# Kernel optimization log

Measured on AMD Instinct MI355X. Metric: run time of the kernel, lower is better.

Reference implementation:

```python
import jax, jax.numpy as jnp
import numpy as np

N, T, D_KQ, E_KQ, D_V, E_V, H = 2, 2048, 1024, 1024, 1024, 1024, 16


def setup_inputs() -> dict:
    key = jax.random.key(0)
    ks = jax.random.split(key, 12)
    def lin(k, fan_in, fan_out):
        return jax.random.normal(k, (fan_in, fan_out), jnp.float32) * (1.0 / np.sqrt(fan_in))
    return {
        "kq": jax.random.normal(ks[0], (N, T, D_KQ), jnp.float32),
        "v": jax.random.normal(ks[1], (N, T, D_V), jnp.float32),
        "Wk": lin(ks[2], D_KQ, E_KQ), "bk": jnp.zeros((E_KQ,), jnp.float32),
        "Wq": lin(ks[3], D_KQ, E_KQ), "bq": jnp.zeros((E_KQ,), jnp.float32),
        "Wv": lin(ks[4], D_V, E_V),   "bv": jnp.zeros((E_V,), jnp.float32),
        "W1": lin(ks[5], E_V, 4 * E_V), "b1": jnp.zeros((4 * E_V,), jnp.float32),
        "W2": lin(ks[6], 4 * E_V, E_V), "b2": jnp.zeros((E_V,), jnp.float32),
    }


def _shifted_causal_mask(T):
    # triu(-inf, diagonal=0): block j >= i (strictly-past attention), except [0,0] unmasked
    row = jnp.arange(T)[:, None]
    col = jnp.arange(T)[None, :]
    mask = jnp.where(col < row, 0.0, -jnp.inf).astype(jnp.float32)
    return mask.at[0, 0].set(0.0)


def reference(kq, v, Wk, bk, Wq, bq, Wv, bv, W1, b1, W2, b2):
    n, T, _ = kq.shape
    hd_kq = E_KQ // H
    hd_v = E_V // H
    # projections -> [n, H, T, hd]
    k = (kq @ Wk + bk).reshape(n, T, H, hd_kq).transpose(0, 2, 1, 3)
    q = (kq @ Wq + bq).reshape(n, T, H, hd_kq).transpose(0, 2, 1, 3)
    vv = (v @ Wv + bv).reshape(n, T, H, hd_v).transpose(0, 2, 1, 3)
    # NOTE: no 1/sqrt(d) scaling, faithful to source
    scores = jnp.einsum("bhqd,bhkd->bhqk", q, k) + _shifted_causal_mask(T)
    attn = jax.nn.softmax(scores, axis=-1)
    out = jnp.einsum("bhqk,bhkd->bhqd", attn, vv)
    out = out.transpose(0, 2, 1, 3).reshape(n, T, E_V)
    # GELU FFN (torch nn.GELU default = exact erf form)
    h = jax.nn.gelu(out @ W1 + b1, approximate=False)
    return h @ W2 + b2
```

## Files before the change

kernel.cpp:

```cpp
#include <hip/hip_runtime.h>

typedef short bf16x8 __attribute__((ext_vector_type(8)));
typedef unsigned short u16x8 __attribute__((ext_vector_type(8)));
typedef float f32x4 __attribute__((ext_vector_type(4)));
typedef unsigned short u16;

#define MFMA16(a, b, c) __builtin_amdgcn_mfma_f32_16x16x32_bf16((a), (b), (c), 0, 0, 0)
#define VMCNT0() asm volatile("s_waitcnt vmcnt(0)" ::: "memory")
#define VMCNTN(n) asm volatile("s_waitcnt vmcnt(" #n ")" ::: "memory")

__device__ __forceinline__ u16 bf16_rtn(float f) {
  unsigned u = __float_as_uint(f);
  u += 0x7fffu + ((u >> 16) & 1u);
  return (u16)(u >> 16);
}
__device__ __forceinline__ float bf16_to_f(u16 h) {
  return __uint_as_float(((unsigned)h) << 16);
}
__device__ __forceinline__ void splitf(float f, u16& hi, u16& lo) {
  hi = bf16_rtn(f);
  lo = bf16_rtn(f - bf16_to_f(hi));
}
__device__ __forceinline__ void gload16(const void* g, void* l) {
  __builtin_amdgcn_global_load_lds(
      (const __attribute__((address_space(1))) unsigned int*)g,
      (__attribute__((address_space(3))) unsigned int*)l, 16, 0, 0);
}
__device__ __forceinline__ float exp2_hw(float x) {
  float r;
  asm("v_exp_f32 %0, %1" : "=v"(r) : "v"(x));
  return r;
}
__device__ __forceinline__ void swz_bid(int& bx, int& by) {
  int gx = gridDim.x;
  int lin = (int)blockIdx.y * gx + (int)blockIdx.x;
  int cpx = (gx * (int)gridDim.y) >> 3;
  int nl = (lin & 7) * cpx + (lin >> 3);
  bx = nl % gx;
  by = nl / gx;
}

__global__ void k_cvt(const float* __restrict__ a, const float* __restrict__ b,
                      u16* __restrict__ ah, u16* __restrict__ vb) {
  int i = blockIdx.x * blockDim.x + threadIdx.x;
  const int N4 = 1 << 20;
  const float4 v4 = (i < N4) ? ((const float4*)a)[i] : ((const float4*)b)[i - N4];
  ushort4 h;
  h.x = bf16_rtn(v4.x);
  h.y = bf16_rtn(v4.y);
  h.z = bf16_rtn(v4.z);
  h.w = bf16_rtn(v4.w);
  if (i < N4)
    ((ushort4*)ah)[i] = h;
  else
    ((ushort4*)vb)[i - N4] = h;
}

__global__ void k_tconvW(const float* __restrict__ Wk, const float* __restrict__ Wq,
                         const float* __restrict__ Wv, u16* __restrict__ hi,
                         u16* __restrict__ lo, u16* __restrict__ wvt) {
  int z = blockIdx.z;
  const float* in = (z == 0) ? Wk : (z == 1) ? Wq : Wv;
  __shared__ float tile[32][33];
  int c0 = blockIdx.x * 32, r0 = blockIdx.y * 32;
  int tx = threadIdx.x & 31, ty = threadIdx.x >> 5;
#pragma unroll
  for (int i = 0; i < 4; ++i)
    tile[ty + i * 8][tx] = in[(size_t)(r0 + ty + i * 8) * 1024 + c0 + tx];
  __syncthreads();
#pragma unroll
  for (int i = 0; i < 4; ++i) {
    float v = tile[tx][ty + i * 8];
    size_t o = (size_t)(c0 + ty + i * 8) * 1024 + r0 + tx;
    if (z < 2) {
      u16 h, l;
      splitf(v, h, l);
      hi[(size_t)z * 1048576 + o] = h;
      lo[(size_t)z * 1048576 + o] = l;
    } else {
      wvt[o] = bf16_rtn(v);
    }
  }
}

__global__ void k_tconv(const float* __restrict__ in, u16* __restrict__ hi,
                        int R, int C) {
  __shared__ float tile[32][33];
  int c0 = blockIdx.x * 32, r0 = blockIdx.y * 32;
  int tx = threadIdx.x & 31, ty = threadIdx.x >> 5;
#pragma unroll
  for (int i = 0; i < 4; ++i)
    tile[ty + i * 8][tx] = in[(size_t)(r0 + ty + i * 8) * C + c0 + tx];
  __syncthreads();
#pragma unroll
  for (int i = 0; i < 4; ++i)
    hi[(size_t)(c0 + ty + i * 8) * R + r0 + tx] = bf16_rtn(tile[tx][ty + i * 8]);
}

template <int GELU, int OUT, int BN>
__global__ __launch_bounds__(256) void k_gemm(
    const u16* __restrict__ A, const u16* __restrict__ B,
    const float* __restrict__ bias, void* __restrict__ C0,
    int M, int Nc, int K) {
  const int NB = BN / 32;
  const int BUFE = 8192 + BN * 64;
  __shared__ u16 sm[3 * BUFE];

  int bx, by;
  swz_bid(bx, by);
  int m0 = by * 128, n0 = bx * BN;
  int t = threadIdx.x, lane = t & 63, w = t >> 6;
  int wr = (w >> 1) * 64, wc = (w & 1) * (BN / 2);
  int li = lane & 15, g = lane >> 4;
  int lrow = lane >> 3, lcg = lane & 7;

  f32x4 acc[4][NB] = {};
  const int nk = K >> 6;

  auto stage = [&](int kb, int buf) {
    int k0 = kb * 64;
    u16* base = sm + buf * BUFE;
#pragma unroll
    for (int j = 0; j < 4; ++j) {
      int jj = w * 4 + j;
      int row = jj * 8 + lrow;
      int cg = lcg ^ (row & 7);
      gload16(A + (size_t)(m0 + row) * K + k0 + cg * 8, base + jj * 512);
    }
#pragma unroll
    for (int j = 0; j < NB; ++j) {
      int jj = w * NB + j;
      int row = jj * 8 + lrow;
      int cg = lcg ^ (row & 7);
      gload16(B + (size_t)(n0 + row) * K + k0 + cg * 8, base + 8192 + jj * 512);
    }
  };

  stage(0, 0);
  stage(1, 1);
  if (NB == 4) { VMCNTN(8); } else { VMCNTN(6); }
  __syncthreads();

  int cur = 0;
  for (int kb = 0; kb < nk; ++kb) {
    int stb = cur + 2;
    if (stb >= 3) stb -= 3;
    if (kb + 2 < nk) stage(kb + 2, stb);

    const u16* bs = sm + cur * BUFE;
#pragma unroll
    for (int kk = 0; kk < 2; ++kk) {
      bf16x8 af[4], bf[NB];
#pragma unroll
      for (int i = 0; i < 4; ++i) {
        int row = wr + i * 16 + li;
        af[i] = *(const bf16x8*)&bs[row * 64 + (((kk * 4 + g) ^ (li & 7)) << 3)];
      }
#pragma unroll
      for (int b = 0; b < NB; ++b) {
        int row = wc + b * 16 + li;
        bf[b] = *(const bf16x8*)&bs[8192 + row * 64 + (((kk * 4 + g) ^ (li & 7)) << 3)];
      }
#pragma unroll
      for (int a = 0; a < 4; ++a)
#pragma unroll
        for (int b = 0; b < NB; ++b) acc[a][b] = MFMA16(af[a], bf[b], acc[a][b]);
    }
    if (kb + 2 < nk) {
      if (NB == 4) { VMCNTN(8); } else { VMCNTN(6); }
    } else {
      VMCNT0();
    }
    __syncthreads();
    cur = (cur == 2) ? 0 : cur + 1;
  }

#pragma unroll
  for (int a = 0; a < 4; ++a)
#pragma unroll
    for (int b = 0; b < NB; ++b)
#pragma unroll
      for (int r = 0; r < 4; ++r) {
        int row = m0 + wr + a * 16 + g * 4 + r;
        int col = n0 + wc + b * 16 + li;
        float v = acc[a][b][r] + bias[col];
        if (GELU) v = 0.5f * v * (1.0f + erff(v * 0.70710678118654752f));
        if (OUT == 0) {
          ((float*)C0)[(size_t)row * Nc + col] = v;
        } else if (OUT == 1) {
          ((u16*)C0)[(size_t)row * Nc + col] = bf16_rtn(v);
        } else if (OUT == 5) {
          int nn = row >> 11, tt = row & 2047, kbb = tt >> 6, tr = tt & 63;
          int hq = col >> 6, d = col & 63;
          size_t base = (((size_t)nn * 16 + hq) * 32 + kbb) * 8192 + 4096;
          size_t ov = base + d * 64 + (tr & 7) + (((tr >> 3) ^ (d & 7)) << 3);
          ((u16*)C0)[ov] = bf16_rtn(v);
        }
      }
}

template <int GELU, int OUT>
__global__ __launch_bounds__(512, 1) void k_gemm2(
    const u16* __restrict__ A, const u16* __restrict__ B,
    const float* __restrict__ bias, void* __restrict__ C0,
    int M, int Nc, int K) {
  const int BUFE = 32768;
  __shared__ u16 sm[2 * BUFE];

  int bx, by;
  swz_bid(bx, by);
  int m0 = by * 256, n0 = bx * 256;
  int t = threadIdx.x, lane = t & 63, w = t >> 6;
  int wr = (w >> 2) * 128, wc = (w & 3) * 64;
  int li = lane & 15, g = lane >> 4;
  int lrow = lane >> 3, lcg = lane & 7;

  f32x4 acc[8][4] = {};
  const int nk = K >> 6;

  auto stage = [&](int kb, int buf) {
    int k0 = kb * 64;
    u16* base = sm + buf * BUFE;
#pragma unroll
    for (int j = 0; j < 4; ++j) {
      int jj = w * 4 + j;
      int row = jj * 8 + lrow;
      int cg = lcg ^ (row & 7);
      gload16(A + (size_t)(m0 + row) * K + k0 + cg * 8, base + jj * 512);
      gload16(B + (size_t)(n0 + row) * K + k0 + cg * 8, base + 16384 + jj * 512);
    }
  };

  stage(0, 0);
  VMCNT0();
  __syncthreads();

  int cur = 0;
  for (int kb = 0; kb < nk; ++kb) {
    if (kb + 1 < nk) stage(kb + 1, cur ^ 1);

    const u16* bs = sm + cur * BUFE;
#pragma unroll
    for (int kk = 0; kk < 2; ++kk) {
      bf16x8 af[8], bf[4];
#pragma unroll
      for (int i = 0; i < 8; ++i) {
        int row = wr + i * 16 + li;
        af[i] = *(const bf16x8*)&bs[row * 64 + (((kk * 4 + g) ^ (li & 7)) << 3)];
      }
#pragma unroll
      for (int b = 0; b < 4; ++b) {
        int row = wc + b * 16 + li;
        bf[b] = *(const bf16x8*)&bs[16384 + row * 64 + (((kk * 4 + g) ^ (li & 7)) << 3)];
      }
#pragma unroll
      for (int a = 0; a < 8; ++a)
#pragma unroll
        for (int b = 0; b < 4; ++b) acc[a][b] = MFMA16(af[a], bf[b], acc[a][b]);
    }
    VMCNT0();
    __syncthreads();
    cur ^= 1;
  }

#pragma unroll
  for (int a = 0; a < 8; ++a)
#pragma unroll
    for (int b = 0; b < 4; ++b)
#pragma unroll
      for (int r = 0; r < 4; ++r) {
        int row = m0 + wr + a * 16 + g * 4 + r;
        int col = n0 + wc + b * 16 + li;
        float v = acc[a][b][r] + bias[col];
        if (GELU) v = 0.5f * v * (1.0f + erff(v * 0.70710678118654752f));
        if (OUT == 1)
          ((u16*)C0)[(size_t)row * Nc + col] = bf16_rtn(v);
        else
          ((float*)C0)[(size_t)row * Nc + col] = v;
      }
}

__global__ __launch_bounds__(256) void k_gemm_s(
    const u16* __restrict__ Ahi, const u16* __restrict__ Bhi,
    const u16* __restrict__ Blo, const float* __restrict__ bias,
    const float* __restrict__ bias2, void* __restrict__ C0,
    void* __restrict__ C1, void* __restrict__ C2, int M, int Nc, int K) {
  const int BUFE = 12288;
  __shared__ u16 sm[3 * BUFE];

  int bx, by;
  swz_bid(bx, by);
  int m0 = by * 128, n0 = bx * 128;
  int t = threadIdx.x, lane = t & 63, w = t >> 6;
  int wr = (w >> 1) * 64, wc = (w & 1) * 64;
  int li = lane & 15, g = lane >> 4;
  int srow = lane >> 2;
  int sc = ((lane & 3) ^ ((srow >> 1) & 3)) * 8;

  f32x4 acc[4][4] = {};
  const int nk = K >> 5;

  auto stage = [&](int kb, int buf) {
    int k0 = kb * 32;
    u16* base = sm + buf * BUFE;
#pragma unroll
    for (int c = 0; c < 2; ++c) {
      int row = w * 32 + c * 16 + srow;
      int ldso = w * 1024 + c * 512;
      gload16(Ahi + (size_t)(m0 + row) * K + k0 + sc, base + ldso);
      gload16(Bhi + (size_t)(n0 + row) * K + k0 + sc, base + 4096 + ldso);
      gload16(Blo + (size_t)(n0 + row) * K + k0 + sc, base + 8192 + ldso);
    }
  };

  stage(0, 0);
  stage(1, 1);
  VMCNTN(6);
  __syncthreads();

  int cur = 0;
  for (int kb = 0; kb < nk; ++kb) {
    int stb = cur + 2;
    if (stb >= 3) stb -= 3;
    if (kb + 2 < nk) stage(kb + 2, stb);

    const u16* bs = sm + cur * BUFE;
    bf16x8 af[4], bfr[4], bfl[4];
#pragma unroll
    for (int i = 0; i < 4; ++i) {
      int swz = (g ^ ((li >> 1) & 3)) << 3;
      af[i] = *(const bf16x8*)&bs[(wr + i * 16 + li) * 32 + swz];
      bfr[i] = *(const bf16x8*)&bs[4096 + (wc + i * 16 + li) * 32 + swz];
      bfl[i] = *(const bf16x8*)&bs[8192 + (wc + i * 16 + li) * 32 + swz];
    }
#pragma unroll
    for (int a = 0; a < 4; ++a)
#pragma unroll
      for (int b = 0; b < 4; ++b) {
        acc[a][b] = MFMA16(af[a], bfr[b], acc[a][b]);
        acc[a][b] = MFMA16(af[a], bfl[b], acc[a][b]);
      }
    if (kb + 2 < nk) {
      VMCNTN(6);
    } else {
      VMCNT0();
    }
    __syncthreads();
    cur = (cur == 2) ? 0 : cur + 1;
  }

#pragma unroll
  for (int a = 0; a < 4; ++a)
#pragma unroll
    for (int b = 0; b < 4; ++b)
#pragma unroll
      for (int r = 0; r < 4; ++r) {
        int row = m0 + wr + a * 16 + g * 4 + r;
        int col = n0 + wc + b * 16 + li;
        float bb = col < 1024 ? bias[col] : bias2[col - 1024];
        float v = acc[a][b][r] + bb;
        if (col < 1024) {
          int nn = row >> 11, tt = row & 2047, kbb = tt >> 6, tr = tt & 63;
          int hq = col >> 6, d = col & 63, ks = d >> 5, dc = d & 31;
          size_t base = (((size_t)nn * 16 + hq) * 32 + kbb) * 8192;
          size_t oh = base + ks * 2048 + tr * 32 + (dc & 7) +
                      (((dc >> 3) ^ ((tr >> 1) & 3)) << 3);
          ((u16*)C0)[oh] = bf16_rtn(v);
        } else {
          int cq = col - 1024;
          float vq = v * 1.4426950408889634f;
          u16 hh, ll;
          splitf(vq, hh, ll);
          size_t off = (((size_t)(row >> 11) * 16 + (cq >> 6)) * 2048 + (row & 2047)) * 64 + (cq & 63);
          ((u16*)C1)[off] = hh;
          ((u16*)C2)[off] = ll;
        }
      }
}

__global__ __launch_bounds__(512) void k_attn(
    const u16* __restrict__ Qh, const u16* __restrict__ Ql,
    const u16* __restrict__ KV, u16* __restrict__ out) {
  const int T = 2048, HD = 64, H = 16, E = 1024;
  int hc = blockIdx.x;
  int h = hc & 15, n = hc >> 4;
  int qq = 15 - (int)blockIdx.y;
  __shared__ u16 KB[3][8192];
  __shared__ u16 P[2][128][36];
  int t = threadIdx.x, lane = t & 63, w = t >> 6;
  int li = lane & 15, g = lane >> 4;

  const size_t nh = (size_t)n * H + h;
  const u16* qhb = Qh + (nh * 2048 + (size_t)qq * 128) * 64;
  const u16* qlb = Ql + (nh * 2048 + (size_t)qq * 128) * 64;
  const u16* kvb = KV + nh * 32 * 8192;

  bf16x8 qh[2], ql[2];
#pragma unroll
  for (int ks = 0; ks < 2; ++ks) {
    qh[ks] = *(const bf16x8*)&qhb[(w * 16 + li) * 64 + ks * 32 + g * 8];
    ql[ks] = *(const bf16x8*)&qlb[(w * 16 + li) * 64 + ks * 32 + g * 8];
  }

#pragma unroll
  for (int j = 0; j < 2; ++j)
    gload16(kvb + (w * 2 + j) * 512 + lane * 8, &KB[0][(w * 2 + j) * 512]);
#pragma unroll
  for (int j = 0; j < 2; ++j)
    gload16(kvb + 8192 + (w * 2 + j) * 512 + lane * 8, &KB[1][(w * 2 + j) * 512]);
  VMCNTN(2);
  __syncthreads();

  float lr[4] = {0.f, 0.f, 0.f, 0.f};
  f32x4 O[4] = {};
  int cur = 0;
  const int nkb = 2 * qq + 2;

  for (int kb = 0; kb < nkb; ++kb) {
    int stb = cur + 2;
    if (stb >= 3) stb -= 3;
    if (kb + 2 < nkb) {
      const u16* src = kvb + (size_t)(kb + 2) * 8192 + (w * 2) * 512 + lane * 8;
#pragma unroll
      for (int j = 0; j < 2; ++j)
        gload16(src + j * 512, &KB[stb][(w * 2 + j) * 512]);
    }

    f32x4 s[4] = {};
#pragma unroll
    for (int ks = 0; ks < 2; ++ks)
#pragma unroll
      for (int c = 0; c < 4; ++c) {
        int jr = c * 16 + li;
        int sw = (jr >> 1) & 3;
        bf16x8 kh = *(const bf16x8*)&KB[cur][ks * 2048 + jr * 32 + ((g ^ sw) << 3)];
        s[c] = MFMA16(qh[ks], kh, s[c]);
        s[c] = MFMA16(ql[ks], kh, s[c]);
      }

    if (kb >= 2 * qq) {
#pragma unroll
      for (int c = 0; c < 4; ++c)
#pragma unroll
        for (int r = 0; r < 4; ++r) {
          int i = qq * 128 + w * 16 + g * 4 + r;
          int j = kb * 64 + c * 16 + li;
          if (!(j < i || (i == 0 && j == 0))) s[c][r] = -INFINITY;
        }
    }

#pragma unroll
    for (int c = 0; c < 4; ++c)
#pragma unroll
      for (int r = 0; r < 4; ++r) {
        float p = exp2_hw(s[c][r]);
        s[c][r] = p;
        lr[r] += p;
      }

#pragma unroll
    for (int c = 0; c < 4; ++c)
#pragma unroll
      for (int r = 0; r < 4; ++r)
        P[c >> 1][w * 16 + g * 4 + r][(c & 1) * 16 + li] = bf16_rtn(s[c][r]);

#pragma unroll
    for (int ks = 0; ks < 2; ++ks) {
      bf16x8 pa = *(const bf16x8*)&P[ks][w * 16 + li][g * 8];
#pragma unroll
      for (int c = 0; c < 4; ++c) {
        int d = c * 16 + li;
        int tc = ks * 4 + g;
        bf16x8 vb = *(const bf16x8*)&KB[cur][4096 + d * 64 + ((tc ^ (d & 7)) << 3)];
        O[c] = MFMA16(pa, vb, O[c]);
      }
    }
    if (kb + 2 < nkb) {
      VMCNTN(2);
    } else {
      VMCNT0();
    }
    __syncthreads();
    cur = (cur == 2) ? 0 : cur + 1;
  }

#pragma unroll
  for (int off = 1; off < 16; off <<= 1)
#pragma unroll
    for (int r = 0; r < 4; ++r) lr[r] += __shfl_xor(lr[r], off, 16);

#pragma unroll
  for (int c = 0; c < 4; ++c)
#pragma unroll
    for (int r = 0; r < 4; ++r) {
      float v = O[c][r] / lr[r];
      size_t row = (size_t)n * T + qq * 128 + w * 16 + g * 4 + r;
      out[row * E + h * HD + c * 16 + li] = bf16_rtn(v);
    }
}

extern "C" void kernel_launch(void* const* d_in, const int* in_sizes, int n_in,
                              void* d_out, int out_size, void* d_ws, size_t ws_size,
                              hipStream_t stream) {
  const float* kq = (const float*)d_in[0];
  const float* v = (const float*)d_in[1];
  const float* Wk = (const float*)d_in[2];
  const float* bk = (const float*)d_in[3];
  const float* Wq = (const float*)d_in[4];
  const float* bq = (const float*)d_in[5];
  const float* Wv = (const float*)d_in[6];
  const float* bv = (const float*)d_in[7];
  const float* W1 = (const float*)d_in[8];
  const float* b1 = (const float*)d_in[9];
  const float* W2 = (const float*)d_in[10];
  const float* b2 = (const float*)d_in[11];
  float* outp = (float*)d_out;

  char* ws = (char*)d_ws;
  u16* kq_hi = (u16*)(ws + 0);
  u16* v_bf = (u16*)(ws + 8388608);
  u16* hbuf = (u16*)(ws + 0);
  u16* WkqT_hi = (u16*)(ws + 33554432);
  u16* WkqT_lo = (u16*)(ws + 37748736);
  u16* WvT = (u16*)(ws + 41943040);
  u16* W1T = (u16*)(ws + 44040192);
  u16* W2T = (u16*)(ws + 52428800);
  u16* Qh = (u16*)(ws + 60817408);
  u16* Ql = (u16*)(ws + 69206016);
  u16* KV = (u16*)(ws + 77594624);
  u16* attn_o = (u16*)(ws + 102760448);

  k_cvt<<<8192, 256, 0, stream>>>(kq, v, kq_hi, v_bf);
  k_tconvW<<<dim3(32, 32, 3), 256, 0, stream>>>(Wk, Wq, Wv, WkqT_hi, WkqT_lo, WvT);
  k_tconv<<<dim3(128, 32), 256, 0, stream>>>(W1, W1T, 1024, 4096);
  k_tconv<<<dim3(32, 128), 256, 0, stream>>>(W2, W2T, 4096, 1024);

  k_gemm_s<<<dim3(16, 32), 256, 0, stream>>>(
      kq_hi, WkqT_hi, WkqT_lo, bk, bq, KV, Qh, Ql, 4096, 2048, 1024);
  k_gemm<0, 5, 64><<<dim3(16, 32), 256, 0, stream>>>(
      v_bf, WvT, bv, KV, 4096, 1024, 1024);

  k_attn<<<dim3(32, 16), 512, 0, stream>>>(Qh, Ql, KV, attn_o);

  k_gemm2<1, 1><<<dim3(16, 16), 512, 0, stream>>>(
      attn_o, W1T, b1, hbuf, 4096, 4096, 1024);
  k_gemm<0, 0, 128><<<dim3(8, 32), 256, 0, stream>>>(
      hbuf, W2T, b2, outp, 4096, 1024, 4096);
}
```

Before: 228.0 us.

## Interleave gemm2 global-to-LDS staging with MFMA phases using barriers and setprio

Splits the next-tile prefetch into four quarter loads issued one per compute phase, and splits each k-step's MFMA work into half-row phases separated by raw s_barrier calls. s_setprio raises wave priority around the MFMA bursts. The aim is to spread memory issue across the compute and let waves overlap loads with matrix math, following the ping-pong style schedule. It adds more barriers per iteration and relies on raw s_barrier without explicit LDS waitcnt, which risks ordering hazards on the ds_reads.

```diff
diff --git a/kernel.cpp b/kernel.cpp
--- a/kernel.cpp
+++ b/kernel.cpp
@@ -218,34 +218,36 @@
   f32x4 acc[8][4] = {};
   const int nk = K >> 6;
 
-  auto stage = [&](int kb, int buf) {
+  auto stageq = [&](int kb, int buf, int q) {
     int k0 = kb * 64;
-    u16* base = sm + buf * BUFE;
-#pragma unroll
-    for (int j = 0; j < 4; ++j) {
-      int jj = w * 4 + j;
+    const u16* src = (q < 2) ? A : B;
+    size_t gr = (size_t)((q < 2) ? m0 : n0) + (q & 1) * 128;
+    u16* nb = sm + buf * BUFE + q * 8192;
+#pragma unroll
+    for (int j = 0; j < 2; ++j) {
+      int jj = w * 2 + j;
       int row = jj * 8 + lrow;
-      int cg = lcg ^ (row & 7);
-      gload16(A + (size_t)(m0 + row) * K + k0 + cg * 8, base + jj * 512);
-      gload16(B + (size_t)(n0 + row) * K + k0 + cg * 8, base + 16384 + jj * 512);
+      int cg = lcg ^ lrow;
+      gload16(src + (gr + row) * K + k0 + cg * 8, nb + jj * 512);
     }
   };
 
-  stage(0, 0);
+#pragma unroll
+  for (int q = 0; q < 4; ++q) stageq(0, 0, q);
   VMCNT0();
-  __syncthreads();
+  __builtin_amdgcn_s_barrier();
 
   int cur = 0;
   for (int kb = 0; kb < nk; ++kb) {
-    if (kb + 1 < nk) stage(kb + 1, cur ^ 1);
-
     const u16* bs = sm + cur * BUFE;
-#pragma unroll
-    for (int kk = 0; kk < 2; ++kk) {
-      bf16x8 af[8], bf[4];
-#pragma unroll
-      for (int i = 0; i < 8; ++i) {
-        int row = wr + i * 16 + li;
+    bool st = (kb + 1 < nk);
+#pragma unroll
+    for (int ph = 0; ph < 4; ++ph) {
+      int h = ph & 1, kk = ph >> 1;
+      bf16x8 af[4], bf[4];
+#pragma unroll
+      for (int i = 0; i < 4; ++i) {
+        int row = wr + (h * 4 + i) * 16 + li;
         af[i] = *(const bf16x8*)&bs[row * 64 + (((kk * 4 + g) ^ (li & 7)) << 3)];
       }
 #pragma unroll
@@ -253,13 +255,18 @@
         int row = wc + b * 16 + li;
         bf[b] = *(const bf16x8*)&bs[16384 + row * 64 + (((kk * 4 + g) ^ (li & 7)) << 3)];
       }
-#pragma unroll
-      for (int a = 0; a < 8; ++a)
-#pragma unroll
-        for (int b = 0; b < 4; ++b) acc[a][b] = MFMA16(af[a], bf[b], acc[a][b]);
-    }
-    VMCNT0();
-    __syncthreads();
+      if (st) stageq(kb + 1, cur ^ 1, ph);
+      __builtin_amdgcn_s_barrier();
+      __builtin_amdgcn_s_setprio(1);
+#pragma unroll
+      for (int a = 0; a < 4; ++a)
+#pragma unroll
+        for (int b = 0; b < 4; ++b)
+          acc[h * 4 + a][b] = MFMA16(af[a], bf[b], acc[h * 4 + a][b]);
+      __builtin_amdgcn_s_setprio(0);
+      if (ph == 3) VMCNT0();
+      __builtin_amdgcn_s_barrier();
+    }
     cur ^= 1;
   }
 
```

Result: no change. 231.5 us (+1.5%).
